# Kernel optimization log

Measured on AMD Instinct MI355X. Metric: run time of the kernel, lower is better.

Reference implementation:

```python
import jax, jax.numpy as jnp
import numpy as np
from jax import lax

EPS = 1e-5  # torch BatchNorm2d default


def setup_inputs() -> dict:
    key = jax.random.key(0)
    k1, k2, k3 = jax.random.split(key, 3)
    C = 64
    x = jax.random.normal(k1, (32, C, 128, 128), dtype=jnp.float32)
    # per-channel 3x3 depthwise weights (OIHW with I=1, feature_group_count=C)
    w = jax.random.normal(k2, (C, 1, 3, 3), dtype=jnp.float32) * (1.0 / 3.0)
    b = jax.random.normal(k3, (C,), dtype=jnp.float32) * 0.1
    gamma = jnp.ones((C,), dtype=jnp.float32)
    beta = jnp.zeros((C,), dtype=jnp.float32)
    return {"x": x, "w": w, "b": b, "gamma": gamma, "beta": beta}


def reference(x, w, b, gamma, beta):
    C = x.shape[1]
    # depthwise 3x3 conv, stride 1, padding 1 (same math as C separate Conv2d(1,1,3))
    y = lax.conv_general_dilated(
        x, w,
        window_strides=(1, 1),
        padding=((1, 1), (1, 1)),
        feature_group_count=C,
        dimension_numbers=("NCHW", "OIHW", "NCHW"),
    )
    y = y + b[None, :, None, None]
    # BatchNorm2d(1) per channel in training mode: batch stats over (N, H, W),
    # biased variance, eps=1e-5
    mean = jnp.mean(y, axis=(0, 2, 3), keepdims=True)
    var = jnp.var(y, axis=(0, 2, 3), keepdims=True)
    y_hat = (y - mean) * lax.rsqrt(var + EPS)
    out = y_hat * gamma[None, :, None, None] + beta[None, :, None, None]
    return jax.nn.relu(out)
```

## Files before the change

### kernel.cpp

```cpp
#include <hip/hip_runtime.h>
#include <hip/hip_cooperative_groups.h>

namespace cg = cooperative_groups;

#define HW        128
#define PLANE     16384
#define NCH       64
#define NB        32
#define NQ        4
#define NPART     8192
#define COUNT_INV (1.0f / 524288.0f)
#define EPSV      1e-5f

#define YELEMS    (NB * NCH * PLANE)
#define PART_OFF  (YELEMS / 2)
#define WS_NEED   ((size_t)YELEMS * 2 + 16384 * 4)

typedef float    f4v __attribute__((ext_vector_type(4)));
typedef _Float16 h2v __attribute__((ext_vector_type(2)));
typedef _Float16 h4v __attribute__((ext_vector_type(4)));

__device__ __forceinline__ void load_win(const float* __restrict__ bp, int r0, int w4,
                                         bool hasL, bool hasR, float (&v)[6][6]) {
#pragma unroll
    for (int i = 0; i < 6; ++i) {
        int g = r0 - 1 + i;
        if ((unsigned)g < (unsigned)HW) {
            const float* rp = bp + g * HW + w4;
            float4 m = *(const float4*)rp;
            v[i][0] = hasL ? rp[-1] : 0.f;
            v[i][1] = m.x; v[i][2] = m.y; v[i][3] = m.z; v[i][4] = m.w;
            v[i][5] = hasR ? rp[4] : 0.f;
        } else {
#pragma unroll
            for (int j = 0; j < 6; ++j) v[i][j] = 0.f;
        }
    }
}

__device__ __forceinline__ void conv_row(const float (&tp)[6], const float (&md)[6],
                                         const float (&bt)[6], const float* W,
                                         float bias, float (&acc)[4]) {
#pragma unroll
    for (int j = 0; j < 4; ++j) {
        float a = bias;
        a = fmaf(tp[j],     W[0], a);
        a = fmaf(tp[j + 1], W[1], a);
        a = fmaf(tp[j + 2], W[2], a);
        a = fmaf(md[j],     W[3], a);
        a = fmaf(md[j + 1], W[4], a);
        a = fmaf(md[j + 2], W[5], a);
        a = fmaf(bt[j],     W[6], a);
        a = fmaf(bt[j + 1], W[7], a);
        a = fmaf(bt[j + 2], W[8], a);
        acc[j] = a;
    }
}

__global__ __launch_bounds__(256, 4) void fused(const float* __restrict__ x,
                                                const float* __restrict__ wgt,
                                                const float* __restrict__ bias,
                                                const float* __restrict__ gamma,
                                                const float* __restrict__ beta,
                                                float* __restrict__ partials,
                                                float* __restrict__ out) {
    __shared__ float red[8];
    __shared__ float ssh[2];
    const int bid = blockIdx.x;
    const int c   = bid & 63;
    const int np  = bid >> 6;
    const int t   = threadIdx.x;
    const int cg_ = t & 31, rg = t >> 5;
    const int w4  = cg_ * 4;
    const bool hasL = (cg_ != 0), hasR = (cg_ != 31);

    float W[9];
#pragma unroll
    for (int k = 0; k < 9; ++k) W[k] = wgt[c * 9 + k];
    const float bv = bias[c];

    h2v y[64];

#pragma unroll
    for (int pp = 0; pp < 2; ++pp) {
        const int n = np * 2 + pp;
        const int plane = n * NCH + c;
        const float* bp = x + (size_t)plane * PLANE;

        float sum = 0.f, sq = 0.f;
#pragma unroll
        for (int k = 0; k < 4; ++k) {
            const int r0 = rg * 16 + k * 4;
            float v[6][6];
            load_win(bp, r0, w4, hasL, hasR, v);
#pragma unroll
            for (int rr = 0; rr < 4; ++rr) {
                float acc[4];
                conv_row(v[rr], v[rr + 1], v[rr + 2], W, bv, acc);
                h2v a, b2;
                a.x  = (_Float16)acc[0]; a.y  = (_Float16)acc[1];
                b2.x = (_Float16)acc[2]; b2.y = (_Float16)acc[3];
                y[pp * 32 + k * 8 + rr * 2]     = a;
                y[pp * 32 + k * 8 + rr * 2 + 1] = b2;
#pragma unroll
                for (int j = 0; j < 4; ++j) {
                    sum += acc[j];
                    sq = fmaf(acc[j], acc[j], sq);
                }
            }
        }
#pragma unroll
        for (int off = 32; off; off >>= 1) {
            sum += __shfl_down(sum, off);
            sq  += __shfl_down(sq, off);
        }
        const int wave = t >> 6, lane = t & 63;
        if (lane == 0) { red[wave] = sum; red[4 + wave] = sq; }
        __syncthreads();
        if (t == 0) {
            partials[c * 32 + n]        = red[0] + red[1] + red[2] + red[3];
            partials[2048 + c * 32 + n] = red[4] + red[5] + red[6] + red[7];
        }
        __syncthreads();
    }

    __threadfence();
    cg::this_grid().sync();

    if (t < 32) {
        float S = partials[c * 32 + t];
        float Q = partials[2048 + c * 32 + t];
#pragma unroll
        for (int off = 16; off; off >>= 1) {
            S += __shfl_xor(S, off);
            Q += __shfl_xor(Q, off);
        }
        if (t == 0) {
            float mean = S * COUNT_INV;
            float var  = fmaxf(Q * COUNT_INV - mean * mean, 0.f);
            float s    = gamma[c] * rsqrtf(var + EPSV);
            ssh[0] = s;
            ssh[1] = beta[c] - mean * s;
        }
    }
    __syncthreads();
    const float s  = ssh[0];
    const float sh = ssh[1];

#pragma unroll
    for (int pp = 0; pp < 2; ++pp) {
        const int plane = (np * 2 + pp) * NCH + c;
        float* op = out + (size_t)plane * PLANE;
#pragma unroll
        for (int k = 0; k < 4; ++k) {
#pragma unroll
            for (int rr = 0; rr < 4; ++rr) {
                h2v a  = y[pp * 32 + k * 8 + rr * 2];
                h2v b2 = y[pp * 32 + k * 8 + rr * 2 + 1];
                f4v o;
                o.x = fmaxf(fmaf((float)a.x,  s, sh), 0.f);
                o.y = fmaxf(fmaf((float)a.y,  s, sh), 0.f);
                o.z = fmaxf(fmaf((float)b2.x, s, sh), 0.f);
                o.w = fmaxf(fmaf((float)b2.y, s, sh), 0.f);
                const int row = rg * 16 + k * 4 + rr;
                __builtin_nontemporal_store(o, (f4v*)(op + row * HW + w4));
            }
        }
    }
}

__global__ __launch_bounds__(256) void pass_conv_stats(const float* __restrict__ x,
                                                       const float* __restrict__ wgt,
                                                       const float* __restrict__ bias,
                                                       _Float16* __restrict__ yh,
                                                       float* __restrict__ partials) {
    __shared__ float red[8];
    const int bid   = blockIdx.x;
    const int q     = bid & 3;
    const int plane = bid >> 2;
    const int c     = plane & 63;
    const int n     = plane >> 6;
    const int t     = threadIdx.x;
    const int cg    = t & 31, rg = t >> 5;
    const int w4    = cg * 4, r0 = q * 32 + rg * 4;
    const bool hasL = (cg != 0), hasR = (cg != 31);

    float W[9];
#pragma unroll
    for (int k = 0; k < 9; ++k) W[k] = wgt[c * 9 + k];
    const float bv = bias[c];
    const float* bp = x + (size_t)plane * PLANE;
    _Float16* yp = yh + (size_t)plane * PLANE;

    float v[6][6];
    load_win(bp, r0, w4, hasL, hasR, v);

    float sum = 0.f, sq = 0.f;
#pragma unroll
    for (int k = 0; k < 4; ++k) {
        float acc[4];
        conv_row(v[k], v[k + 1], v[k + 2], W, bv, acc);
        h4v hv;
        hv.x = (_Float16)acc[0]; hv.y = (_Float16)acc[1];
        hv.z = (_Float16)acc[2]; hv.w = (_Float16)acc[3];
        *(h4v*)(yp + (r0 + k) * HW + w4) = hv;
#pragma unroll
        for (int j = 0; j < 4; ++j) { sum += acc[j]; sq = fmaf(acc[j], acc[j], sq); }
    }
#pragma unroll
    for (int off = 32; off; off >>= 1) {
        sum += __shfl_down(sum, off);
        sq  += __shfl_down(sq, off);
    }
    const int wave = t >> 6, lane = t & 63;
    if (lane == 0) { red[wave] = sum; red[4 + wave] = sq; }
    __syncthreads();
    if (t == 0) {
        const int pi = n * 4 + q;
        partials[c * 128 + pi]         = red[0] + red[1] + red[2] + red[3];
        partials[NPART + c * 128 + pi] = red[4] + red[5] + red[6] + red[7];
    }
}

__global__ __launch_bounds__(256) void pass_norm(const _Float16* __restrict__ yh,
                                                 const float* __restrict__ partials,
                                                 const float* __restrict__ gamma,
                                                 const float* __restrict__ beta,
                                                 float* __restrict__ out) {
    const int bid   = blockIdx.x;
    const int q     = bid & 3;
    const int plane = bid >> 2;
    const int c     = plane & 63;
    const int t     = threadIdx.x;
    const int cg    = t & 31, rg = t >> 5;
    const int w4    = cg * 4, r0 = q * 32 + rg * 4;

    const _Float16* yp = yh + (size_t)plane * PLANE;
    h4v hv[4];
#pragma unroll
    for (int k = 0; k < 4; ++k)
        hv[k] = *(const h4v*)(yp + (r0 + k) * HW + w4);

    const int lane = t & 63;
    float S = partials[c * 128 + lane]         + partials[c * 128 + 64 + lane];
    float Q = partials[NPART + c * 128 + lane] + partials[NPART + c * 128 + 64 + lane];
#pragma unroll
    for (int off = 32; off; off >>= 1) {
        S += __shfl_xor(S, off);
        Q += __shfl_xor(Q, off);
    }
    const float mean = S * COUNT_INV;
    const float var  = fmaxf(Q * COUNT_INV - mean * mean, 0.f);
    const float s    = gamma[c] * rsqrtf(var + EPSV);
    const float sh   = beta[c] - mean * s;

    float* op = out + (size_t)plane * PLANE;
#pragma unroll
    for (int k = 0; k < 4; ++k) {
        f4v o;
        o.x = fmaxf(fmaf((float)hv[k].x, s, sh), 0.f);
        o.y = fmaxf(fmaf((float)hv[k].y, s, sh), 0.f);
        o.z = fmaxf(fmaf((float)hv[k].z, s, sh), 0.f);
        o.w = fmaxf(fmaf((float)hv[k].w, s, sh), 0.f);
        __builtin_nontemporal_store(o, (f4v*)(op + (r0 + k) * HW + w4));
    }
}

extern "C" void kernel_launch(void* const* d_in, const int* in_sizes, int n_in,
                              void* d_out, int out_size, void* d_ws, size_t ws_size,
                              hipStream_t stream) {
    const float* x     = (const float*)d_in[0];
    const float* w     = (const float*)d_in[1];
    const float* b     = (const float*)d_in[2];
    const float* gamma = (const float*)d_in[3];
    const float* beta  = (const float*)d_in[4];
    float* out = (float*)d_out;

    int nb = 0;
    hipError_t qe = hipOccupancyMaxActiveBlocksPerMultiprocessor(
        &nb, reinterpret_cast<const void*>(fused), 256, 0);

    if (qe == hipSuccess && nb >= 4) {
        float* parts = (float*)d_ws;
        const float* xa = x; const float* wa = w; const float* ba = b;
        const float* ga = gamma; const float* be = beta;
        float* pw = parts; float* oa = out;
        void* args[] = {&xa, &wa, &ba, &ga, &be, &pw, &oa};
        hipLaunchCooperativeKernel(reinterpret_cast<const void*>(fused),
                                   dim3(1024), dim3(256), args, 0, stream);
    } else if (ws_size >= WS_NEED) {
        _Float16* yh  = (_Float16*)d_ws;
        float* parts  = (float*)d_ws + PART_OFF;
        pass_conv_stats<<<NB * NCH * NQ, 256, 0, stream>>>(x, w, b, yh, parts);
        pass_norm<<<NB * NCH * NQ, 256, 0, stream>>>(yh, parts, gamma, beta, out);
    }
}
```

Before: 72.94 us.

## Process four planes per block with half the cooperative grid

The fused cooperative kernel now has each block handle four batch planes instead of two. The conv results for each plane are held in registers as 64-wide fp16 vectors, and the grid is halved to 512 blocks with launch bounds of 2 blocks per CU. The intent is fewer blocks and less grid-sync overhead, with more work per thread. In exchange register pressure doubles and occupancy drops, which may hurt latency hiding for the memory-bound conv.

```diff
diff --git a/kernel.cpp b/kernel.cpp
--- a/kernel.cpp
+++ b/kernel.cpp
@@ -16,9 +16,9 @@
 #define PART_OFF  (YELEMS / 2)
 #define WS_NEED   ((size_t)YELEMS * 2 + 16384 * 4)
 
-typedef float    f4v __attribute__((ext_vector_type(4)));
-typedef _Float16 h2v __attribute__((ext_vector_type(2)));
-typedef _Float16 h4v __attribute__((ext_vector_type(4)));
+typedef float    f4v  __attribute__((ext_vector_type(4)));
+typedef _Float16 h4v  __attribute__((ext_vector_type(4)));
+typedef _Float16 h64v __attribute__((ext_vector_type(64)));
 
 __device__ __forceinline__ void load_win(const float* __restrict__ bp, int r0, int w4,
                                          bool hasL, bool hasR, float (&v)[6][6]) {
@@ -57,7 +57,67 @@
     }
 }
 
-__global__ __launch_bounds__(256, 4) void fused(const float* __restrict__ x,
+
+#define PHASE1(PI, Y)                                                          \
+    {                                                                          \
+        const int n     = np4 + (PI);                                          \
+        const int plane = n * NCH + c;                                         \
+        const float* bp = x + (size_t)plane * PLANE;                           \
+        float sum = 0.f, sq = 0.f;                                             \
+        _Pragma("unroll")                                                      \
+        for (int k = 0; k < 4; ++k) {                                          \
+            const int r0 = rg * 16 + k * 4;                                    \
+            float v[6][6];                                                     \
+            load_win(bp, r0, w4, hasL, hasR, v);                               \
+            _Pragma("unroll")                                                  \
+            for (int rr = 0; rr < 4; ++rr) {                                   \
+                float acc[4];                                                  \
+                conv_row(v[rr], v[rr + 1], v[rr + 2], W, bv, acc);             \
+                Y[k * 16 + rr * 4 + 0] = (_Float16)acc[0];                     \
+                Y[k * 16 + rr * 4 + 1] = (_Float16)acc[1];                     \
+                Y[k * 16 + rr * 4 + 2] = (_Float16)acc[2];                     \
+                Y[k * 16 + rr * 4 + 3] = (_Float16)acc[3];                     \
+                _Pragma("unroll")                                              \
+                for (int j = 0; j < 4; ++j) {                                  \
+                    sum += acc[j];                                             \
+                    sq = fmaf(acc[j], acc[j], sq);                             \
+                }                                                              \
+            }                                                                  \
+        }                                                                      \
+        _Pragma("unroll")                                                      \
+        for (int off = 32; off; off >>= 1) {                                   \
+            sum += __shfl_down(sum, off);                                      \
+            sq  += __shfl_down(sq, off);                                       \
+        }                                                                      \
+        if ((t & 63) == 0) { red[t >> 6] = sum; red[4 + (t >> 6)] = sq; }      \
+        __syncthreads();                                                       \
+        if (t == 0) {                                                          \
+            partials[c * 32 + n]        = red[0] + red[1] + red[2] + red[3];   \
+            partials[2048 + c * 32 + n] = red[4] + red[5] + red[6] + red[7];   \
+        }                                                                      \
+        __syncthreads();                                                       \
+    }
+
+#define PHASE2(PI, Y)                                                          \
+    {                                                                          \
+        const int plane = (np4 + (PI)) * NCH + c;                              \
+        float* op = out + (size_t)plane * PLANE;                               \
+        _Pragma("unroll")                                                      \
+        for (int k = 0; k < 4; ++k) {                                          \
+            _Pragma("unroll")                                                  \
+            for (int rr = 0; rr < 4; ++rr) {                                   \
+                f4v o;                                                         \
+                o.x = fmaxf(fmaf((float)Y[k * 16 + rr * 4 + 0], s, sh), 0.f);  \
+                o.y = fmaxf(fmaf((float)Y[k * 16 + rr * 4 + 1], s, sh), 0.f);  \
+                o.z = fmaxf(fmaf((float)Y[k * 16 + rr * 4 + 2], s, sh), 0.f);  \
+                o.w = fmaxf(fmaf((float)Y[k * 16 + rr * 4 + 3], s, sh), 0.f);  \
+                const int row = rg * 16 + k * 4 + rr;                          \
+                __builtin_nontemporal_store(o, (f4v*)(op + row * HW + w4));    \
+            }                                                                  \
+        }                                                                      \
+    }
+
+__global__ __launch_bounds__(256, 2) void fused(const float* __restrict__ x,
                                                 const float* __restrict__ wgt,
                                                 const float* __restrict__ bias,
                                                 const float* __restrict__ gamma,
@@ -68,7 +128,7 @@
     __shared__ float ssh[2];
     const int bid = blockIdx.x;
     const int c   = bid & 63;
-    const int np  = bid >> 6;
+    const int np4 = (bid >> 6) * 4;
     const int t   = threadIdx.x;
     const int cg_ = t & 31, rg = t >> 5;
     const int w4  = cg_ * 4;
@@ -79,50 +139,12 @@
     for (int k = 0; k < 9; ++k) W[k] = wgt[c * 9 + k];
     const float bv = bias[c];
 
-    h2v y[64];
-
-#pragma unroll
-    for (int pp = 0; pp < 2; ++pp) {
-        const int n = np * 2 + pp;
-        const int plane = n * NCH + c;
-        const float* bp = x + (size_t)plane * PLANE;
-
-        float sum = 0.f, sq = 0.f;
-#pragma unroll
-        for (int k = 0; k < 4; ++k) {
-            const int r0 = rg * 16 + k * 4;
-            float v[6][6];
-            load_win(bp, r0, w4, hasL, hasR, v);
-#pragma unroll
-            for (int rr = 0; rr < 4; ++rr) {
-                float acc[4];
-                conv_row(v[rr], v[rr + 1], v[rr + 2], W, bv, acc);
-                h2v a, b2;
-                a.x  = (_Float16)acc[0]; a.y  = (_Float16)acc[1];
-                b2.x = (_Float16)acc[2]; b2.y = (_Float16)acc[3];
-                y[pp * 32 + k * 8 + rr * 2]     = a;
-                y[pp * 32 + k * 8 + rr * 2 + 1] = b2;
-#pragma unroll
-                for (int j = 0; j < 4; ++j) {
-                    sum += acc[j];
-                    sq = fmaf(acc[j], acc[j], sq);
-                }
-            }
-        }
-#pragma unroll
-        for (int off = 32; off; off >>= 1) {
-            sum += __shfl_down(sum, off);
-            sq  += __shfl_down(sq, off);
-        }
-        const int wave = t >> 6, lane = t & 63;
-        if (lane == 0) { red[wave] = sum; red[4 + wave] = sq; }
-        __syncthreads();
-        if (t == 0) {
-            partials[c * 32 + n]        = red[0] + red[1] + red[2] + red[3];
-            partials[2048 + c * 32 + n] = red[4] + red[5] + red[6] + red[7];
-        }
-        __syncthreads();
-    }
+    h64v yA, yB, yC, yD;
+
+    PHASE1(0, yA)
+    PHASE1(1, yB)
+    PHASE1(2, yC)
+    PHASE1(3, yD)
 
     __threadfence();
     cg::this_grid().sync();
@@ -147,26 +169,10 @@
     const float s  = ssh[0];
     const float sh = ssh[1];
 
-#pragma unroll
-    for (int pp = 0; pp < 2; ++pp) {
-        const int plane = (np * 2 + pp) * NCH + c;
-        float* op = out + (size_t)plane * PLANE;
-#pragma unroll
-        for (int k = 0; k < 4; ++k) {
-#pragma unroll
-            for (int rr = 0; rr < 4; ++rr) {
-                h2v a  = y[pp * 32 + k * 8 + rr * 2];
-                h2v b2 = y[pp * 32 + k * 8 + rr * 2 + 1];
-                f4v o;
-                o.x = fmaxf(fmaf((float)a.x,  s, sh), 0.f);
-                o.y = fmaxf(fmaf((float)a.y,  s, sh), 0.f);
-                o.z = fmaxf(fmaf((float)b2.x, s, sh), 0.f);
-                o.w = fmaxf(fmaf((float)b2.y, s, sh), 0.f);
-                const int row = rg * 16 + k * 4 + rr;
-                __builtin_nontemporal_store(o, (f4v*)(op + row * HW + w4));
-            }
-        }
-    }
+    PHASE2(0, yA)
+    PHASE2(1, yB)
+    PHASE2(2, yC)
+    PHASE2(3, yD)
 }
 
 __global__ __launch_bounds__(256) void pass_conv_stats(const float* __restrict__ x,
@@ -280,14 +286,14 @@
     hipError_t qe = hipOccupancyMaxActiveBlocksPerMultiprocessor(
         &nb, reinterpret_cast<const void*>(fused), 256, 0);
 
-    if (qe == hipSuccess && nb >= 4) {
+    if (qe == hipSuccess && nb >= 2) {
         float* parts = (float*)d_ws;
         const float* xa = x; const float* wa = w; const float* ba = b;
         const float* ga = gamma; const float* be = beta;
         float* pw = parts; float* oa = out;
         void* args[] = {&xa, &wa, &ba, &ga, &be, &pw, &oa};
         hipLaunchCooperativeKernel(reinterpret_cast<const void*>(fused),
-                                   dim3(1024), dim3(256), args, 0, stream);
+                                   dim3(512), dim3(256), args, 0, stream);
     } else if (ws_size >= WS_NEED) {
         _Float16* yh  = (_Float16*)d_ws;
         float* parts  = (float*)d_ws + PART_OFF;
```

Result: no change. 72.88 us (-0.1%).

## Recompute depthwise conv after grid barrier instead of holding fp16 results in registers

Applied to the files above, without the earlier changes.

The fused cooperative kernel no longer keeps the conv output as fp16 in 64 registers across the grid sync. After the barrier it re-reads x and recomputes the 3x3 conv, folding the bias into the BN shift. Block-to-plane mapping changes to two consecutive planes per block. The cg grid sync is replaced by a hand-rolled atomic counter barrier with sleep polling, which needs a memset launch first. Window halos now come from wave shuffles instead of extra scalar loads. This trades a second read of x (likely partly cached) for lower register pressure and no fp16 rounding of y.

```diff
diff --git a/kernel.cpp b/kernel.cpp
--- a/kernel.cpp
+++ b/kernel.cpp
@@ -1,7 +1,4 @@
 #include <hip/hip_runtime.h>
-#include <hip/hip_cooperative_groups.h>
-
-namespace cg = cooperative_groups;
 
 #define HW        128
 #define PLANE     16384
@@ -11,13 +8,13 @@
 #define NPART     8192
 #define COUNT_INV (1.0f / 524288.0f)
 #define EPSV      1e-5f
+#define GRID_C    1024
 
 #define YELEMS    (NB * NCH * PLANE)
 #define PART_OFF  (YELEMS / 2)
 #define WS_NEED   ((size_t)YELEMS * 2 + 16384 * 4)
 
 typedef float    f4v __attribute__((ext_vector_type(4)));
-typedef _Float16 h2v __attribute__((ext_vector_type(2)));
 typedef _Float16 h4v __attribute__((ext_vector_type(4)));
 
 __device__ __forceinline__ void load_win(const float* __restrict__ bp, int r0, int w4,
@@ -25,16 +22,14 @@
 #pragma unroll
     for (int i = 0; i < 6; ++i) {
         int g = r0 - 1 + i;
-        if ((unsigned)g < (unsigned)HW) {
-            const float* rp = bp + g * HW + w4;
-            float4 m = *(const float4*)rp;
-            v[i][0] = hasL ? rp[-1] : 0.f;
-            v[i][1] = m.x; v[i][2] = m.y; v[i][3] = m.z; v[i][4] = m.w;
-            v[i][5] = hasR ? rp[4] : 0.f;
-        } else {
-#pragma unroll
-            for (int j = 0; j < 6; ++j) v[i][j] = 0.f;
-        }
+        float4 m = make_float4(0.f, 0.f, 0.f, 0.f);
+        if ((unsigned)g < (unsigned)HW)
+            m = *(const float4*)(bp + g * HW + w4);
+        float l = __shfl_up(m.w, 1);
+        float r = __shfl_down(m.x, 1);
+        v[i][0] = hasL ? l : 0.f;
+        v[i][1] = m.x; v[i][2] = m.y; v[i][3] = m.z; v[i][4] = m.w;
+        v[i][5] = hasR ? r : 0.f;
     }
 }
 
@@ -63,45 +58,37 @@
                                                 const float* __restrict__ gamma,
                                                 const float* __restrict__ beta,
                                                 float* __restrict__ partials,
+                                                unsigned int* __restrict__ cnt,
                                                 float* __restrict__ out) {
     __shared__ float red[8];
-    __shared__ float ssh[2];
-    const int bid = blockIdx.x;
-    const int c   = bid & 63;
-    const int np  = bid >> 6;
+    __shared__ float ssh[4];
+    const int b   = blockIdx.x;
     const int t   = threadIdx.x;
     const int cg_ = t & 31, rg = t >> 5;
     const int w4  = cg_ * 4;
     const bool hasL = (cg_ != 0), hasR = (cg_ != 31);
 
-    float W[9];
-#pragma unroll
-    for (int k = 0; k < 9; ++k) W[k] = wgt[c * 9 + k];
-    const float bv = bias[c];
-
-    h2v y[64];
-
 #pragma unroll
     for (int pp = 0; pp < 2; ++pp) {
-        const int n = np * 2 + pp;
-        const int plane = n * NCH + c;
+        const int plane = b * 2 + pp;
+        const int c = plane & 63, n = plane >> 6;
         const float* bp = x + (size_t)plane * PLANE;
 
+        float W[9];
+#pragma unroll
+        for (int k = 0; k < 9; ++k) W[k] = wgt[c * 9 + k];
+        const float bv = bias[c];
+
         float sum = 0.f, sq = 0.f;
 #pragma unroll
-        for (int k = 0; k < 4; ++k) {
-            const int r0 = rg * 16 + k * 4;
+        for (int q = 0; q < 4; ++q) {
+            const int r0 = q * 32 + rg * 4;
             float v[6][6];
             load_win(bp, r0, w4, hasL, hasR, v);
 #pragma unroll
-            for (int rr = 0; rr < 4; ++rr) {
+            for (int k = 0; k < 4; ++k) {
                 float acc[4];
-                conv_row(v[rr], v[rr + 1], v[rr + 2], W, bv, acc);
-                h2v a, b2;
-                a.x  = (_Float16)acc[0]; a.y  = (_Float16)acc[1];
-                b2.x = (_Float16)acc[2]; b2.y = (_Float16)acc[3];
-                y[pp * 32 + k * 8 + rr * 2]     = a;
-                y[pp * 32 + k * 8 + rr * 2 + 1] = b2;
+                conv_row(v[k], v[k + 1], v[k + 2], W, bv, acc);
 #pragma unroll
                 for (int j = 0; j < 4; ++j) {
                     sum += acc[j];
@@ -114,8 +101,7 @@
             sum += __shfl_down(sum, off);
             sq  += __shfl_down(sq, off);
         }
-        const int wave = t >> 6, lane = t & 63;
-        if (lane == 0) { red[wave] = sum; red[4 + wave] = sq; }
+        if ((t & 63) == 0) { red[t >> 6] = sum; red[4 + (t >> 6)] = sq; }
         __syncthreads();
         if (t == 0) {
             partials[c * 32 + n]        = red[0] + red[1] + red[2] + red[3];
@@ -124,47 +110,101 @@
         __syncthreads();
     }
 
-    __threadfence();
-    cg::this_grid().sync();
-
-    if (t < 32) {
-        float S = partials[c * 32 + t];
-        float Q = partials[2048 + c * 32 + t];
-#pragma unroll
-        for (int off = 16; off; off >>= 1) {
-            S += __shfl_xor(S, off);
-            Q += __shfl_xor(Q, off);
-        }
-        if (t == 0) {
-            float mean = S * COUNT_INV;
-            float var  = fmaxf(Q * COUNT_INV - mean * mean, 0.f);
-            float s    = gamma[c] * rsqrtf(var + EPSV);
-            ssh[0] = s;
-            ssh[1] = beta[c] - mean * s;
+    if (t == 0) {
+        __threadfence();
+        __hip_atomic_fetch_add(cnt, 1u, __ATOMIC_ACQ_REL, __HIP_MEMORY_SCOPE_AGENT);
+        while (__hip_atomic_load(cnt, __ATOMIC_ACQUIRE, __HIP_MEMORY_SCOPE_AGENT)
+               < (unsigned)GRID_C) {
+            __builtin_amdgcn_s_sleep(8);
         }
     }
     __syncthreads();
-    const float s  = ssh[0];
-    const float sh = ssh[1];
+
+    {
+        const int c0 = (b * 2) & 63;
+        const int c1 = (b * 2 + 1) & 63;
+        if (t < 32) {
+            float S = partials[c0 * 32 + t];
+            float Q = partials[2048 + c0 * 32 + t];
+#pragma unroll
+            for (int off = 16; off; off >>= 1) {
+                S += __shfl_xor(S, off);
+                Q += __shfl_xor(Q, off);
+            }
+            if (t == 0) {
+                float mean = S * COUNT_INV;
+                float var  = fmaxf(Q * COUNT_INV - mean * mean, 0.f);
+                float s    = gamma[c0] * rsqrtf(var + EPSV);
+                ssh[0] = s;
+                ssh[1] = beta[c0] - mean * s;
+            }
+        } else if (t >= 64 && t < 96) {
+            const int l = t - 64;
+            float S = partials[c1 * 32 + l];
+            float Q = partials[2048 + c1 * 32 + l];
+#pragma unroll
+            for (int off = 16; off; off >>= 1) {
+                S += __shfl_xor(S, off);
+                Q += __shfl_xor(Q, off);
+            }
+            if (l == 0) {
+                float mean = S * COUNT_INV;
+                float var  = fmaxf(Q * COUNT_INV - mean * mean, 0.f);
+                float s    = gamma[c1] * rsqrtf(var + EPSV);
+                ssh[2] = s;
+                ssh[3] = beta[c1] - mean * s;
+            }
+        }
+    }
+    __syncthreads();
 
 #pragma unroll
     for (int pp = 0; pp < 2; ++pp) {
-        const int plane = (np * 2 + pp) * NCH + c;
+        const int plane = b * 2 + pp;
+        const int c = plane & 63;
+        const float* bp = x + (size_t)plane * PLANE;
         float* op = out + (size_t)plane * PLANE;
-#pragma unroll
-        for (int k = 0; k < 4; ++k) {
-#pragma unroll
-            for (int rr = 0; rr < 4; ++rr) {
-                h2v a  = y[pp * 32 + k * 8 + rr * 2];
-                h2v b2 = y[pp * 32 + k * 8 + rr * 2 + 1];
+
+        float W[9];
+#pragma unroll
+        for (int k = 0; k < 9; ++k) W[k] = wgt[c * 9 + k];
+        const float s  = ssh[pp * 2];
+        const float sh = fmaf(bias[c], s, ssh[pp * 2 + 1]);
+
+#pragma unroll
+        for (int q = 0; q < 4; ++q) {
+            const int r0 = q * 32 + rg * 4;
+            float v[6][6];
+            load_win(bp, r0, w4, hasL, hasR, v);
+#pragma unroll
+            for (int k = 0; k < 4; ++k) {
+                float acc[4];
+                conv_row(v[k], v[k + 1], v[k + 2], W, 0.f, acc);
                 f4v o;
-                o.x = fmaxf(fmaf((float)a.x,  s, sh), 0.f);
-                o.y = fmaxf(fmaf((float)a.y,  s, sh), 0.f);
-                o.z = fmaxf(fmaf((float)b2.x, s, sh), 0.f);
-                o.w = fmaxf(fmaf((float)b2.y, s, sh), 0.f);
-                const int row = rg * 16 + k * 4 + rr;
-                __builtin_nontemporal_store(o, (f4v*)(op + row * HW + w4));
-            }
+                o.x = fmaxf(fmaf(acc[0], s, sh), 0.f);
+                o.y = fmaxf(fmaf(acc[1], s, sh), 0.f);
+                o.z = fmaxf(fmaf(acc[2], s, sh), 0.f);
+                o.w = fmaxf(fmaf(acc[3], s, sh), 0.f);
+                __builtin_nontemporal_store(o, (f4v*)(op + (r0 + k) * HW + w4));
+            }
+        }
+    }
+}
+
+__device__ __forceinline__ void load_win_fb(const float* __restrict__ bp, int r0, int w4,
+                                            bool hasL, bool hasR, float (&v)[6][6]) {
+#pragma unroll
+    for (int i = 0; i < 6; ++i) {
+        int g = r0 - 1 + i;
+        if ((unsigned)g < (unsigned)HW) {
+            const float* rp = bp + g * HW + w4;
+            float4 m = *(const float4*)rp;
+            v[i][0] = hasL ? rp[-1] : 0.f;
+            v[i][1] = m.x; v[i][2] = m.y; v[i][3] = m.z; v[i][4] = m.w;
+            v[i][5] = hasR ? rp[4] : 0.f;
+        } else {
+#pragma unroll
+            for (int j = 0; j < 6; ++j) v[i][j] = 0.f;
         }
     }
 }
@@ -193,7 +233,7 @@
     _Float16* yp = yh + (size_t)plane * PLANE;
 
     float v[6][6];
-    load_win(bp, r0, w4, hasL, hasR, v);
+    load_win_fb(bp, r0, w4, hasL, hasR, v);
 
     float sum = 0.f, sq = 0.f;
 #pragma unroll
@@ -280,15 +320,22 @@
     hipError_t qe = hipOccupancyMaxActiveBlocksPerMultiprocessor(
         &nb, reinterpret_cast<const void*>(fused), 256, 0);
 
+    bool coop_ok = false;
     if (qe == hipSuccess && nb >= 4) {
-        float* parts = (float*)d_ws;
+        float* parts      = (float*)d_ws;
+        unsigned int* cnt = (unsigned int*)((float*)d_ws + 4096);
+        hipMemsetAsync(cnt, 0, sizeof(unsigned int), stream);
         const float* xa = x; const float* wa = w; const float* ba = b;
         const float* ga = gamma; const float* be = beta;
-        float* pw = parts; float* oa = out;
-        void* args[] = {&xa, &wa, &ba, &ga, &be, &pw, &oa};
-        hipLaunchCooperativeKernel(reinterpret_cast<const void*>(fused),
-                                   dim3(1024), dim3(256), args, 0, stream);
-    } else if (ws_size >= WS_NEED) {
+        float* pw = parts; unsigned int* ca = cnt; float* oa = out;
+        void* args[] = {&xa, &wa, &ba, &ga, &be, &pw, &ca, &oa};
+        hipError_t le = hipLaunchCooperativeKernel(
+            reinterpret_cast<const void*>(fused), dim3(GRID_C), dim3(256),
+            args, 0, stream);
+        coop_ok = (le == hipSuccess);
+    }
+
+    if (!coop_ok && ws_size >= WS_NEED) {
         _Float16* yh  = (_Float16*)d_ws;
         float* parts  = (float*)d_ws + PART_OFF;
         pass_conv_stats<<<NB * NCH * NQ, 256, 0, stream>>>(x, w, b, yh, parts);
```

Measured after the change: 73.01 us. About the same (+0.1%).
